# Kernel optimization log

Measured on AMD Instinct MI355X. Metric: run time of the kernel, lower is better.

The kernel has to match this reference:

```python
import jax, jax.numpy as jnp
import numpy as np

B, S1, S2 = 16, 256, 512          # batch, vision len, text len
V_HID, T_HID = 1024, 768          # v_hidden_size, hidden_size
BI_HID, H = 1024, 8               # bi_hidden_size, bi_num_attention_heads
D = BI_HID // H                   # attention_head_size = 128


def setup_inputs() -> dict:
    key = jax.random.key(0)
    ks = jax.random.split(key, 16)
    s = 0.02
    inp = {
        "input_tensor1": jax.random.normal(ks[0], (B, S1, V_HID), jnp.float32),
        "attention_mask1": jnp.zeros((B, 1, 1, S1), jnp.float32),
        "input_tensor2": jax.random.normal(ks[1], (B, S2, T_HID), jnp.float32),
        "attention_mask2": jnp.zeros((B, 1, 1, S2), jnp.float32),
        # vision-stream projections (query1/key1/value1): v_hidden -> all_head_size
        "Wq1": jax.random.normal(ks[2], (V_HID, BI_HID), jnp.float32) * s,
        "bq1": jnp.zeros((BI_HID,), jnp.float32),
        "Wk1": jax.random.normal(ks[3], (V_HID, BI_HID), jnp.float32) * s,
        "bk1": jnp.zeros((BI_HID,), jnp.float32),
        "Wv1": jax.random.normal(ks[4], (V_HID, BI_HID), jnp.float32) * s,
        "bv1": jnp.zeros((BI_HID,), jnp.float32),
        # text-stream projections (query2/key2/value2): hidden -> all_head_size
        "Wq2": jax.random.normal(ks[5], (T_HID, BI_HID), jnp.float32) * s,
        "bq2": jnp.zeros((BI_HID,), jnp.float32),
        "Wk2": jax.random.normal(ks[6], (T_HID, BI_HID), jnp.float32) * s,
        "bk2": jnp.zeros((BI_HID,), jnp.float32),
        "Wv2": jax.random.normal(ks[7], (T_HID, BI_HID), jnp.float32) * s,
        "bv2": jnp.zeros((BI_HID,), jnp.float32),
    }
    return inp


def _heads(x):
    # [B, S, H*D] -> [B, S, H, D]
    b, s, _ = x.shape
    return x.reshape(b, s, H, D)


def reference(input_tensor1, attention_mask1, input_tensor2, attention_mask2,
              Wq1, bq1, Wk1, bk1, Wv1, bv1,
              Wq2, bq2, Wk2, bk2, Wv2, bv2):
    scale = 1.0 / jnp.sqrt(jnp.asarray(D, input_tensor1.dtype))
    # stream 1 (vision) QKV
    q1 = _heads(input_tensor1 @ Wq1 + bq1)
    k1 = _heads(input_tensor1 @ Wk1 + bk1)
    v1 = _heads(input_tensor1 @ Wv1 + bv1)
    # stream 2 (text) QKV
    q2 = _heads(input_tensor2 @ Wq2 + bq2)
    k2 = _heads(input_tensor2 @ Wk2 + bk2)
    v2 = _heads(input_tensor2 @ Wv2 + bv2)

    # attention 1: text queries attend to vision keys/values  -> context1 [B,S2,BI_HID]
    scores1 = jnp.einsum('bqhd,bkhd->bhqk', q2, k1) * scale + attention_mask1
    probs1 = jax.nn.softmax(scores1, axis=-1)  # dropout prob = 0 (eval)
    context1 = jnp.einsum('bhqk,bkhd->bqhd', probs1, v1).reshape(B, S2, BI_HID)

    # attention 2: vision queries attend to text keys/values  -> context2 [B,S1,BI_HID]
    scores2 = jnp.einsum('bqhd,bkhd->bhqk', q1, k2) * scale + attention_mask2
    probs2 = jax.nn.softmax(scores2, axis=-1)
    context2 = jnp.einsum('bhqk,bkhd->bqhd', probs2, v2).reshape(B, S1, BI_HID)

    return (context1, context2)
```

## Files before the change

kernel.cpp:

```cpp
#include <hip/hip_runtime.h>


typedef _Float16 f16;
typedef unsigned int u32;
typedef f16  v8h __attribute__((ext_vector_type(8)));
typedef float v4f __attribute__((ext_vector_type(4)));

struct alignas(8) h4 { f16 x, y, z, w; };

#define GLL16(g, l) __builtin_amdgcn_global_load_lds(                          \
    (const __attribute__((address_space(1))) u32*)(g),                         \
    (__attribute__((address_space(3))) u32*)(l), 16, 0, 0)

#define MFMA16 __builtin_amdgcn_mfma_f32_16x16x32_f16

__global__ __launch_bounds__(256)
void cvt_in(const float* __restrict__ p1, long n1,
            const float* __restrict__ p2, long n2,
            f16* __restrict__ d1, f16* __restrict__ d2)
{
    long i = ((long)blockIdx.x * 256 + threadIdx.x) * 8;
    const float* s; f16* d;
    if (i < n1) { s = p1 + i; d = d1 + i; }
    else        { long j = i - n1; if (j >= n2) return; s = p2 + j; d = d2 + j; }
    float4 a = *(const float4*)s, b = *(const float4*)(s + 4);
    v8h o = {(f16)a.x, (f16)a.y, (f16)a.z, (f16)a.w,
             (f16)b.x, (f16)b.y, (f16)b.z, (f16)b.w};
    *(v8h*)d = o;
}

__global__ __launch_bounds__(256)
void cvt_wT(const float* __restrict__ w0, const float* __restrict__ w1,
            const float* __restrict__ w2, const float* __restrict__ w3,
            const float* __restrict__ w4, const float* __restrict__ w5,
            f16* __restrict__ o1, f16* __restrict__ o2)
{
    const int z = blockIdx.z;
    const int K = z < 3 ? 1024 : 768;
    const int bk = blockIdx.y * 64;
    if (bk >= K) return;
    const float* src = z == 0 ? w0 : z == 1 ? w1 : z == 2 ? w2
                     : z == 3 ? w3 : z == 4 ? w4 : w5;
    f16* dst = z < 3 ? o1 + (size_t)z * 1024 * 1024
                     : o2 + (size_t)(z - 3) * 1024 * 768;

    __shared__ float t[64][65];
    const int bn = blockIdx.x * 64;
    const int r0 = threadIdx.x >> 4, c4 = (threadIdx.x & 15) * 4;
#pragma unroll
    for (int rr = 0; rr < 64; rr += 16) {
        float4 v = *(const float4*)&src[(long)(bk + rr + r0) * 1024 + bn + c4];
        t[rr + r0][c4 + 0] = v.x; t[rr + r0][c4 + 1] = v.y;
        t[rr + r0][c4 + 2] = v.z; t[rr + r0][c4 + 3] = v.w;
    }
    __syncthreads();
#pragma unroll
    for (int rr = 0; rr < 64; rr += 16) {
        const int n = rr + r0;
        h4 o = {(f16)t[c4 + 0][n], (f16)t[c4 + 1][n],
                (f16)t[c4 + 2][n], (f16)t[c4 + 3][n]};
        *(h4*)&dst[(long)(bn + n) * K + bk + c4] = o;
    }
}

__global__ __launch_bounds__(256, 4)
void mm_proj(const f16* __restrict__ A2, const f16* __restrict__ B2,
             const float* __restrict__ bq2, const float* __restrict__ bk2,
             const float* __restrict__ bv2,
             f16* __restrict__ q2o, f16* __restrict__ k2o, f16* __restrict__ v2o,
             const f16* __restrict__ A1, const f16* __restrict__ B1,
             const float* __restrict__ bq1, const float* __restrict__ bk1,
             const float* __restrict__ bv1,
             f16* __restrict__ q1o, f16* __restrict__ k1o, f16* __restrict__ v1o)
{
    __shared__ f16 sh[16384];

    const int gid = blockIdx.x;
    const bool is2 = gid < 1536;
    const int id   = is2 ? gid : gid - 1536;
    const int K    = is2 ? 768 : 1024;
    const int S    = is2 ? 512 : 256;
    const int mdiv = is2 ? 8 : 4;
    const f16* A  = is2 ? A2 : A1;
    const f16* Bw = is2 ? B2 : B1;

    const int by = (id & 7) * mdiv + ((id >> 3) % mdiv);
    const int bx = id / (8 * mdiv);
    const int m0 = by * 128, n0 = bx * 128;

    const int tid = threadIdx.x, lane = tid & 63, w = tid >> 6;
    const int wm = w >> 1, wn = w & 1;
    const int fr = lane & 15, fq = lane >> 4;

    int aoff[4], boff[4];
#pragma unroll
    for (int t = 0; t < 4; ++t) {
        const int ra = wm * 64 + t * 16 + fr;
        aoff[t] = ra * 32 + (fq ^ ((ra >> 1) & 3)) * 8;
        const int rb = wn * 64 + t * 16 + fr;
        boff[t] = rb * 32 + (fq ^ ((rb >> 1) & 3)) * 8;
    }

    auto stage = [&](int k0, int p) {
        f16* Ad = sh + p * 4096;
        f16* Bd = sh + 8192 + p * 4096;
#pragma unroll
        for (int j = 0; j < 2; ++j) {
            const int c = j * 256 + tid, row = c >> 2;
            const int kl = (c & 3) ^ ((row >> 1) & 3);
            GLL16(A  + (long)(m0 + row) * K + k0 + kl * 8, Ad + c * 8);
            GLL16(Bw + (long)(n0 + row) * K + k0 + kl * 8, Bd + c * 8);
        }
    };

    v4f acc[4][4];
#pragma unroll
    for (int i = 0; i < 4; ++i)
#pragma unroll
        for (int j = 0; j < 4; ++j) acc[i][j] = (v4f){0.f, 0.f, 0.f, 0.f};

    stage(0, 0);
    const int NK = K >> 5;
    for (int kt = 0; kt < NK; ++kt) {
        __syncthreads();
        if (kt + 1 < NK) stage((kt + 1) << 5, (kt + 1) & 1);
        const f16* As = sh + (kt & 1) * 4096;
        const f16* Bs = sh + 8192 + (kt & 1) * 4096;
        v8h ah[4], bh[4];
#pragma unroll
        for (int t = 0; t < 4; ++t) ah[t] = *(const v8h*)&As[aoff[t]];
#pragma unroll
        for (int t = 0; t < 4; ++t) bh[t] = *(const v8h*)&Bs[boff[t]];
#pragma unroll
        for (int tmi = 0; tmi < 4; ++tmi)
#pragma unroll
            for (int tni = 0; tni < 4; ++tni)
                acc[tmi][tni] = MFMA16(ah[tmi], bh[tni], acc[tmi][tni], 0, 0, 0);
    }

    const int col = lane & 15, quad = lane >> 4;
    const int seg = n0 >> 10, nbase = n0 & 1023;
    f16* buf = sh;

    if (seg < 2) {
        const float* bias = seg == 0 ? (is2 ? bq2 : bq1) : (is2 ? bk2 : bk1);
        f16* Co = seg == 0 ? (is2 ? q2o : q1o) : (is2 ? k2o : k1o);
#pragma unroll
        for (int pass = 0; pass < 2; ++pass) {
            __syncthreads();
            if (wm == pass) {
#pragma unroll
                for (int tmi = 0; tmi < 4; ++tmi) {
                    const int ml = tmi * 16 + quad * 4;
#pragma unroll
                    for (int tni = 0; tni < 4; ++tni) {
                        const int nl = wn * 64 + tni * 16 + col;
                        const float bvl = bias[nbase + nl];
#pragma unroll
                        for (int i = 0; i < 4; ++i)
                            buf[(ml + i) * 136 + nl] = (f16)(acc[tmi][tni][i] + bvl);
                    }
                }
            }
            __syncthreads();
            const int rr = tid >> 2, cc = (tid & 3) * 32;
            const long gb = (long)(m0 + pass * 64 + rr) * 1024 + nbase + cc;
#pragma unroll
            for (int c = 0; c < 4; ++c)
                *(v8h*)&Co[gb + c * 8] = *(const v8h*)&buf[rr * 136 + cc + c * 8];
        }
    } else {
        const float* bias = is2 ? bv2 : bv1;
        f16* vo = is2 ? v2o : v1o;
        const int bb = m0 / S, s0 = m0 % S;
#pragma unroll
        for (int pass = 0; pass < 2; ++pass) {
            __syncthreads();
            if (wn == pass) {
#pragma unroll
                for (int tmi = 0; tmi < 4; ++tmi) {
                    const int ml = wm * 64 + tmi * 16 + quad * 4;
#pragma unroll
                    for (int tni = 0; tni < 4; ++tni) {
                        const int nl = tni * 16 + col;
                        const float bvl = bias[nbase + pass * 64 + nl];
                        h4 o = {(f16)(acc[tmi][tni][0] + bvl),
                                (f16)(acc[tmi][tni][1] + bvl),
                                (f16)(acc[tmi][tni][2] + bvl),
                                (f16)(acc[tmi][tni][3] + bvl)};
                        *(h4*)&buf[nl * 136 + ml] = o;
                    }
                }
            }
            __syncthreads();
            const int nn = tid >> 2, mm = (tid & 3) * 32;
            const long gb = ((long)bb * 1024 + nbase + pass * 64 + nn) * S + s0 + mm;
#pragma unroll
            for (int c = 0; c < 4; ++c)
                *(v8h*)&vo[gb + c * 8] = *(const v8h*)&buf[nn * 136 + mm + c * 8];
        }
    }
}

__global__ __launch_bounds__(256, 2)
void flash(const f16* __restrict__ q2, const f16* __restrict__ k1,
           const f16* __restrict__ v1, const float* __restrict__ m1,
           float* __restrict__ o1,
           const f16* __restrict__ q1, const f16* __restrict__ k2,
           const f16* __restrict__ v2, const float* __restrict__ m2,
           float* __restrict__ o2, float scale)
{
    constexpr int PSTR = 72;
    __shared__ f16 lds[16384 + 128 * PSTR];
    f16* KL = lds;
    f16* VL = lds + 8192;
    f16* PL = lds + 16384;

    const int gid = blockIdx.x;
    const bool ph2 = gid < 256;
    const int id = ph2 ? gid : gid - 256;
    const int Sq = ph2 ? 256 : 512, Sk = ph2 ? 512 : 256;
    const f16* qp = ph2 ? q1 : q2;
    const f16* kp = ph2 ? k2 : k1;
    const f16* vp = ph2 ? v2 : v1;
    const float* mask = ph2 ? m2 : m1;
    float* out = ph2 ? o2 : o1;

    const int zz = id & 127, yy = id >> 7;
    const int b = zz >> 3, hd = zz & 7;
    const int q0 = yy * 128;
    const int tid = threadIdx.x, lane = tid & 63, w = tid >> 6;
    const int col = lane & 15, quad = lane >> 4;

    v8h qf[2][4];
#pragma unroll
    for (int rt = 0; rt < 2; ++rt) {
        const long qr = ((long)b * Sq + q0 + w * 32 + rt * 16 + col) * 1024
                        + (long)hd * 128;
#pragma unroll
        for (int kf = 0; kf < 4; ++kf)
            qf[rt][kf] = *(const v8h*)(qp + qr + kf * 32 + quad * 8);
    }

    v8h ones;
#pragma unroll
    for (int i = 0; i < 8; ++i) ones[i] = (f16)1.0f;

    v4f O[2][8], Lc[2];
#pragma unroll
    for (int rt = 0; rt < 2; ++rt) {
#pragma unroll
        for (int nj = 0; nj < 8; ++nj) O[rt][nj] = (v4f){0.f, 0.f, 0.f, 0.f};
        Lc[rt] = (v4f){0.f, 0.f, 0.f, 0.f};
    }

    const long kbase = (long)b * Sk * 1024 + (long)hd * 128;
    const long vbase = ((long)b * 1024 + hd * 128) * (long)Sk;
    const int nk = Sk >> 6;

    auto stageK = [&](int kt) {
#pragma unroll
        for (int j = 0; j < 4; ++j) {
            const int c = j * 256 + tid, row = c >> 4, ch = (c & 15) ^ (row & 15);
            GLL16(kp + kbase + (long)(kt * 64 + row) * 1024 + ch * 8, KL + c * 8);
        }
    };
    auto stageV = [&](int kt) {
#pragma unroll
        for (int j = 0; j < 4; ++j) {
            const int c = j * 256 + tid, row = c >> 3, ch = (c & 7) ^ (row & 7);
            GLL16(vp + vbase + (long)row * Sk + kt * 64 + ch * 8, VL + c * 8);
        }
    };

    stageK(0);
    stageV(0);

    float mv[4];
#pragma unroll
    for (int tn = 0; tn < 4; ++tn)
        mv[tn] = mask[(long)b * Sk + tn * 16 + col];

    for (int kt = 0; kt < nk; ++kt) {
        asm volatile("s_waitcnt vmcnt(4)" ::: "memory");
        __builtin_amdgcn_sched_barrier(0);
        __builtin_amdgcn_s_barrier();

        v4f sa[2][4];
#pragma unroll
        for (int rt = 0; rt < 2; ++rt)
#pragma unroll
            for (int tn = 0; tn < 4; ++tn) sa[rt][tn] = (v4f){0.f, 0.f, 0.f, 0.f};
#pragma unroll
        for (int kf = 0; kf < 4; ++kf) {
            v8h bh[4];
#pragma unroll
            for (int tn = 0; tn < 4; ++tn) {
                const int row = tn * 16 + col;
                bh[tn] = *(const v8h*)&KL[row * 128 + ((kf * 4 + quad) ^ (row & 15)) * 8];
            }
            __builtin_amdgcn_s_setprio(1);
#pragma unroll
            for (int rt = 0; rt < 2; ++rt)
#pragma unroll
                for (int tn = 0; tn < 4; ++tn)
                    sa[rt][tn] = MFMA16(qf[rt][kf], bh[tn], sa[rt][tn], 0, 0, 0);
            __builtin_amdgcn_s_setprio(0);
        }

        float mvn[4];
        if (kt + 1 < nk) {
#pragma unroll
            for (int tn = 0; tn < 4; ++tn)
                mvn[tn] = mask[(long)b * Sk + (kt + 1) * 64 + tn * 16 + col];
        }

        asm volatile("s_waitcnt lgkmcnt(0)" ::: "memory");
        __builtin_amdgcn_sched_barrier(0);
        __builtin_amdgcn_s_barrier();
        if (kt + 1 < nk) stageK(kt + 1);

#pragma unroll
        for (int rt = 0; rt < 2; ++rt)
#pragma unroll
            for (int tn = 0; tn < 4; ++tn)
#pragma unroll
                for (int r = 0; r < 4; ++r) {
                    const float p = __expf(sa[rt][tn][r] * scale + mv[tn]);
                    PL[(w * 32 + rt * 16 + quad * 4 + r) * PSTR + tn * 16 + col]
                        = (f16)p;
                }

        if (kt + 1 < nk) asm volatile("s_waitcnt vmcnt(4)" ::: "memory");
        else             asm volatile("s_waitcnt vmcnt(0)" ::: "memory");
        __builtin_amdgcn_sched_barrier(0);
        __builtin_amdgcn_s_barrier();

#pragma unroll
        for (int kf2 = 0; kf2 < 2; ++kf2) {
            v8h vb[8];
#pragma unroll
            for (int nj = 0; nj < 8; ++nj) {
                const int row = nj * 16 + col;
                vb[nj] = *(const v8h*)&VL[row * 64 + ((kf2 * 4 + quad) ^ (row & 7)) * 8];
            }
#pragma unroll
            for (int rt = 0; rt < 2; ++rt) {
                const v8h pa = *(const v8h*)&PL[(w * 32 + rt * 16 + col) * PSTR
                                                + kf2 * 32 + quad * 8];
                __builtin_amdgcn_s_setprio(1);
#pragma unroll
                for (int nj = 0; nj < 8; ++nj)
                    O[rt][nj] = MFMA16(pa, vb[nj], O[rt][nj], 0, 0, 0);
                Lc[rt] = MFMA16(pa, ones, Lc[rt], 0, 0, 0);
                __builtin_amdgcn_s_setprio(0);
            }
        }

        asm volatile("s_waitcnt lgkmcnt(0)" ::: "memory");
        __builtin_amdgcn_sched_barrier(0);
        __builtin_amdgcn_s_barrier();
        if (kt + 1 < nk) stageV(kt + 1);

#pragma unroll
        for (int tn = 0; tn < 4; ++tn) mv[tn] = mvn[tn];
    }

#pragma unroll
    for (int rt = 0; rt < 2; ++rt) {
        float inv[4];
#pragma unroll
        for (int r = 0; r < 4; ++r) inv[r] = 1.0f / Lc[rt][r];
        const long ob = ((long)b * Sq + q0 + w * 32 + rt * 16 + quad * 4) * 1024
                        + (long)hd * 128;
#pragma unroll
        for (int nj = 0; nj < 8; ++nj)
#pragma unroll
            for (int r = 0; r < 4; ++r)
                out[ob + (long)r * 1024 + nj * 16 + col] = O[rt][nj][r] * inv[r];
    }
}

extern "C" void kernel_launch(void* const* d_in, const int* in_sizes, int n_in,
                              void* d_out, int out_size, void* d_ws, size_t ws_size,
                              hipStream_t stream)
{
    const float* in1   = (const float*)d_in[0];
    const float* mask1 = (const float*)d_in[1];
    const float* in2   = (const float*)d_in[2];
    const float* mask2 = (const float*)d_in[3];
    const float* Wq1 = (const float*)d_in[4];  const float* bq1 = (const float*)d_in[5];
    const float* Wk1 = (const float*)d_in[6];  const float* bk1 = (const float*)d_in[7];
    const float* Wv1 = (const float*)d_in[8];  const float* bv1 = (const float*)d_in[9];
    const float* Wq2 = (const float*)d_in[10]; const float* bq2 = (const float*)d_in[11];
    const float* Wk2 = (const float*)d_in[12]; const float* bk2 = (const float*)d_in[13];
    const float* Wv2 = (const float*)d_in[14]; const float* bv2 = (const float*)d_in[15];

    constexpr int Bb = 16, S1 = 256, S2 = 512, VH = 1024, TH = 768;
    constexpr long M1 = (long)Bb * S1, M2 = (long)Bb * S2;
    const float scale = 0.088388347648318447f;

    f16* W = (f16*)d_ws;
    f16* i1  = W;
    f16* i2  = i1 + M1 * VH;
    f16* w1  = i2 + M2 * TH;
    f16* w2  = w1 + (long)3072 * VH;
    f16* q1  = w2 + (long)3072 * TH;
    f16* k1  = q1 + M1 * 1024;
    f16* v1t = k1 + M1 * 1024;
    f16* q2  = v1t + M1 * 1024;
    f16* k2  = q2 + M2 * 1024;
    f16* v2t = k2 + M2 * 1024;
    float* out = (float*)d_out;

    cvt_in<<<dim3(5120), 256, 0, stream>>>(in1, M1 * VH, in2, M2 * TH, i1, i2);
    cvt_wT<<<dim3(16, 16, 6), 256, 0, stream>>>(Wq1, Wk1, Wv1, Wq2, Wk2, Wv2, w1, w2);

    mm_proj<<<dim3(2304), 256, 0, stream>>>(
        i2, w2, bq2, bk2, bv2, q2, k2, v2t,
        i1, w1, bq1, bk1, bv1, q1, k1, v1t);

    flash<<<dim3(768), 256, 0, stream>>>(
        q2, k1, v1t, mask1, out,
        q1, k2, v2t, mask2, out + M2 * 1024, scale);
}
```

Measured before the change: 252.5 us.

## Enlarge projection GEMM tile to 256x128, single-buffer LDS, merge conversion kernels

The two fp32-to-fp16 conversion kernels (inputs and transposed weights) are merged into one launch, dispatching on block index. The projection GEMM tile grows from 128x128 to 256x128, giving each warp 8x4 MFMA accumulators and halving the block count. LDS staging moves from double-buffered to single-buffered with a sync before compute. The intent is more operand reuse per tile and one fewer launch, but the change also gives up load/compute overlap and raises register pressure.

Measured after the change: 602.0 us. 2.38x slower.

```diff
diff --git a/kernel.cpp b/kernel.cpp
--- a/kernel.cpp
+++ b/kernel.cpp
@@ -15,37 +15,39 @@
 #define MFMA16 __builtin_amdgcn_mfma_f32_16x16x32_f16
 
 __global__ __launch_bounds__(256)
-void cvt_in(const float* __restrict__ p1, long n1,
-            const float* __restrict__ p2, long n2,
-            f16* __restrict__ d1, f16* __restrict__ d2)
+void cvt_all(const float* __restrict__ p1, long n1,
+             const float* __restrict__ p2, long n2,
+             f16* __restrict__ d1, f16* __restrict__ d2,
+             const float* __restrict__ w0, const float* __restrict__ w1,
+             const float* __restrict__ w2, const float* __restrict__ w3,
+             const float* __restrict__ w4, const float* __restrict__ w5,
+             f16* __restrict__ o1, f16* __restrict__ o2)
 {
-    long i = ((long)blockIdx.x * 256 + threadIdx.x) * 8;
-    const float* s; f16* d;
-    if (i < n1) { s = p1 + i; d = d1 + i; }
-    else        { long j = i - n1; if (j >= n2) return; s = p2 + j; d = d2 + j; }
-    float4 a = *(const float4*)s, b = *(const float4*)(s + 4);
-    v8h o = {(f16)a.x, (f16)a.y, (f16)a.z, (f16)a.w,
-             (f16)b.x, (f16)b.y, (f16)b.z, (f16)b.w};
-    *(v8h*)d = o;
-}
-
-__global__ __launch_bounds__(256)
-void cvt_wT(const float* __restrict__ w0, const float* __restrict__ w1,
-            const float* __restrict__ w2, const float* __restrict__ w3,
-            const float* __restrict__ w4, const float* __restrict__ w5,
-            f16* __restrict__ o1, f16* __restrict__ o2)
-{
-    const int z = blockIdx.z;
+    __shared__ float t[64][65];
+    const int bid = blockIdx.x;
+    if (bid < 5120) {
+        long i = ((long)bid * 256 + threadIdx.x) * 8;
+        const float* s; f16* d;
+        if (i < n1) { s = p1 + i; d = d1 + i; }
+        else        { long j = i - n1; if (j >= n2) return; s = p2 + j; d = d2 + j; }
+        float4 a = *(const float4*)s, b = *(const float4*)(s + 4);
+        v8h o = {(f16)a.x, (f16)a.y, (f16)a.z, (f16)a.w,
+                 (f16)b.x, (f16)b.y, (f16)b.z, (f16)b.w};
+        *(v8h*)d = o;
+        return;
+    }
+    const int id = bid - 5120;
+    const int z = id >> 8;
+    const int rem = id & 255;
     const int K = z < 3 ? 1024 : 768;
-    const int bk = blockIdx.y * 64;
+    const int bk = (rem >> 4) * 64;
     if (bk >= K) return;
     const float* src = z == 0 ? w0 : z == 1 ? w1 : z == 2 ? w2
                      : z == 3 ? w3 : z == 4 ? w4 : w5;
     f16* dst = z < 3 ? o1 + (size_t)z * 1024 * 1024
                      : o2 + (size_t)(z - 3) * 1024 * 768;
 
-    __shared__ float t[64][65];
-    const int bn = blockIdx.x * 64;
+    const int bn = (rem & 15) * 64;
     const int r0 = threadIdx.x >> 4, c4 = (threadIdx.x & 15) * 4;
 #pragma unroll
     for (int rr = 0; rr < 64; rr += 16) {
@@ -64,140 +66,145 @@
 }
 
 __global__ __launch_bounds__(256, 4)
-void mm_proj(const f16* __restrict__ A2, const f16* __restrict__ B2,
+void mm_proj(const f16* __restrict__ A1, const f16* __restrict__ B1,
+             const float* __restrict__ bq1, const float* __restrict__ bk1,
+             const float* __restrict__ bv1,
+             f16* __restrict__ q1o, f16* __restrict__ k1o, f16* __restrict__ v1o,
+             const f16* __restrict__ A2, const f16* __restrict__ B2,
              const float* __restrict__ bq2, const float* __restrict__ bk2,
              const float* __restrict__ bv2,
-             f16* __restrict__ q2o, f16* __restrict__ k2o, f16* __restrict__ v2o,
-             const f16* __restrict__ A1, const f16* __restrict__ B1,
-             const float* __restrict__ bq1, const float* __restrict__ bk1,
-             const float* __restrict__ bv1,
-             f16* __restrict__ q1o, f16* __restrict__ k1o, f16* __restrict__ v1o)
+             f16* __restrict__ q2o, f16* __restrict__ k2o, f16* __restrict__ v2o)
 {
-    __shared__ f16 sh[16384];
+    __shared__ f16 sh[17408];
 
     const int gid = blockIdx.x;
-    const bool is2 = gid < 1536;
-    const int id   = is2 ? gid : gid - 1536;
-    const int K    = is2 ? 768 : 1024;
-    const int S    = is2 ? 512 : 256;
-    const int mdiv = is2 ? 8 : 4;
-    const f16* A  = is2 ? A2 : A1;
-    const f16* Bw = is2 ? B2 : B1;
-
-    const int by = (id & 7) * mdiv + ((id >> 3) % mdiv);
-    const int bx = id / (8 * mdiv);
-    const int m0 = by * 128, n0 = bx * 128;
+    const bool is1 = gid < 384;
+    const int id   = is1 ? gid : gid - 384;
+    const int K    = is1 ? 1024 : 768;
+    const int S    = is1 ? 256 : 512;
+    int by, bx;
+    if (is1) { by = (id & 7) * 2 + ((id >> 3) & 1); bx = id >> 4; }
+    else     { by = (id & 7) * 4 + ((id >> 3) & 3); bx = id >> 5; }
+    const int m0 = by << 8, n0 = bx << 7;
+    const f16* A  = is1 ? A1 : A2;
+    const f16* Bw = is1 ? B1 : B2;
 
     const int tid = threadIdx.x, lane = tid & 63, w = tid >> 6;
     const int wm = w >> 1, wn = w & 1;
     const int fr = lane & 15, fq = lane >> 4;
 
-    int aoff[4], boff[4];
-#pragma unroll
-    for (int t = 0; t < 4; ++t) {
-        const int ra = wm * 64 + t * 16 + fr;
-        aoff[t] = ra * 32 + (fq ^ ((ra >> 1) & 3)) * 8;
-        const int rb = wn * 64 + t * 16 + fr;
-        boff[t] = rb * 32 + (fq ^ ((rb >> 1) & 3)) * 8;
-    }
-
-    auto stage = [&](int k0, int p) {
-        f16* Ad = sh + p * 4096;
-        f16* Bd = sh + 8192 + p * 4096;
+    int aoff[8], boff[4];
+#pragma unroll
+    for (int mi = 0; mi < 8; ++mi) {
+        const int ra = wm * 128 + mi * 16 + fr;
+        aoff[mi] = ra * 32 + (fq ^ ((ra >> 1) & 3)) * 8;
+    }
+#pragma unroll
+    for (int n = 0; n < 4; ++n) {
+        const int rb = wn * 64 + n * 16 + fr;
+        boff[n] = rb * 32 + (fq ^ ((rb >> 1) & 3)) * 8;
+    }
+
+    auto stage = [&](int k0) {
+#pragma unroll
+        for (int j = 0; j < 4; ++j) {
+            const int c = j * 256 + tid, row = c >> 2;
+            const int kl = (c & 3) ^ ((row >> 1) & 3);
+            GLL16(A + (long)(m0 + row) * K + k0 + kl * 8, sh + c * 8);
+        }
 #pragma unroll
         for (int j = 0; j < 2; ++j) {
             const int c = j * 256 + tid, row = c >> 2;
             const int kl = (c & 3) ^ ((row >> 1) & 3);
-            GLL16(A  + (long)(m0 + row) * K + k0 + kl * 8, Ad + c * 8);
-            GLL16(Bw + (long)(n0 + row) * K + k0 + kl * 8, Bd + c * 8);
+            GLL16(Bw + (long)(n0 + row) * K + k0 + kl * 8, sh + 8192 + c * 8);
         }
     };
 
-    v4f acc[4][4];
-#pragma unroll
-    for (int i = 0; i < 4; ++i)
+    v4f acc[8][4];
+#pragma unroll
+    for (int i = 0; i < 8; ++i)
 #pragma unroll
         for (int j = 0; j < 4; ++j) acc[i][j] = (v4f){0.f, 0.f, 0.f, 0.f};
 
-    stage(0, 0);
     const int NK = K >> 5;
     for (int kt = 0; kt < NK; ++kt) {
         __syncthreads();
-        if (kt + 1 < NK) stage((kt + 1) << 5, (kt + 1) & 1);
-        const f16* As = sh + (kt & 1) * 4096;
-        const f16* Bs = sh + 8192 + (kt & 1) * 4096;
-        v8h ah[4], bh[4];
-#pragma unroll
-        for (int t = 0; t < 4; ++t) ah[t] = *(const v8h*)&As[aoff[t]];
-#pragma unroll
-        for (int t = 0; t < 4; ++t) bh[t] = *(const v8h*)&Bs[boff[t]];
-#pragma unroll
-        for (int tmi = 0; tmi < 4; ++tmi)
-#pragma unroll
-            for (int tni = 0; tni < 4; ++tni)
-                acc[tmi][tni] = MFMA16(ah[tmi], bh[tni], acc[tmi][tni], 0, 0, 0);
-    }
-
-    const int col = lane & 15, quad = lane >> 4;
+        stage(kt << 5);
+        __syncthreads();
+        v8h bh[4];
+#pragma unroll
+        for (int n = 0; n < 4; ++n) bh[n] = *(const v8h*)&sh[8192 + boff[n]];
+#pragma unroll
+        for (int mi = 0; mi < 8; ++mi) {
+            const v8h ah = *(const v8h*)&sh[aoff[mi]];
+#pragma unroll
+            for (int n = 0; n < 4; ++n)
+                acc[mi][n] = MFMA16(ah, bh[n], acc[mi][n], 0, 0, 0);
+        }
+    }
+
+    const int col = fr, quad = lane >> 4;
     const int seg = n0 >> 10, nbase = n0 & 1023;
     f16* buf = sh;
 
     if (seg < 2) {
-        const float* bias = seg == 0 ? (is2 ? bq2 : bq1) : (is2 ? bk2 : bk1);
-        f16* Co = seg == 0 ? (is2 ? q2o : q1o) : (is2 ? k2o : k1o);
+        const float* bias = seg == 0 ? (is1 ? bq1 : bq2) : (is1 ? bk1 : bk2);
+        f16* Co = seg == 0 ? (is1 ? q1o : q2o) : (is1 ? k1o : k2o);
+        float bl[4];
+#pragma unroll
+        for (int n = 0; n < 4; ++n) bl[n] = bias[nbase + wn * 64 + n * 16 + col];
 #pragma unroll
         for (int pass = 0; pass < 2; ++pass) {
             __syncthreads();
             if (wm == pass) {
 #pragma unroll
-                for (int tmi = 0; tmi < 4; ++tmi) {
-                    const int ml = tmi * 16 + quad * 4;
-#pragma unroll
-                    for (int tni = 0; tni < 4; ++tni) {
-                        const int nl = wn * 64 + tni * 16 + col;
-                        const float bvl = bias[nbase + nl];
+                for (int mi = 0; mi < 8; ++mi) {
+                    const int ml = mi * 16 + quad * 4;
+#pragma unroll
+                    for (int n = 0; n < 4; ++n) {
+                        const int nl = wn * 64 + n * 16 + col;
 #pragma unroll
                         for (int i = 0; i < 4; ++i)
-                            buf[(ml + i) * 136 + nl] = (f16)(acc[tmi][tni][i] + bvl);
+                            buf[(ml + i) * 136 + nl] = (f16)(acc[mi][n][i] + bl[n]);
                     }
                 }
             }
             __syncthreads();
-            const int rr = tid >> 2, cc = (tid & 3) * 32;
-            const long gb = (long)(m0 + pass * 64 + rr) * 1024 + nbase + cc;
-#pragma unroll
-            for (int c = 0; c < 4; ++c)
+            const int rr = tid >> 1, cc = (tid & 1) * 64;
+            const long gb = (long)(m0 + pass * 128 + rr) * 1024 + nbase + cc;
+#pragma unroll
+            for (int c = 0; c < 8; ++c)
                 *(v8h*)&Co[gb + c * 8] = *(const v8h*)&buf[rr * 136 + cc + c * 8];
         }
     } else {
-        const float* bias = is2 ? bv2 : bv1;
-        f16* vo = is2 ? v2o : v1o;
+        const float* bias = is1 ? bv1 : bv2;
+        f16* vo = is1 ? v1o : v2o;
         const int bb = m0 / S, s0 = m0 % S;
 #pragma unroll
         for (int pass = 0; pass < 2; ++pass) {
             __syncthreads();
             if (wn == pass) {
 #pragma unroll
-                for (int tmi = 0; tmi < 4; ++tmi) {
-                    const int ml = wm * 64 + tmi * 16 + quad * 4;
-#pragma unroll
-                    for (int tni = 0; tni < 4; ++tni) {
-                        const int nl = tni * 16 + col;
+                for (int mi = 0; mi < 8; ++mi) {
+                    const int ml = wm * 128 + mi * 16 + quad * 4;
+#pragma unroll
+                    for (int n = 0; n < 4; ++n) {
+                        const int nl = n * 16 + col;
                         const float bvl = bias[nbase + pass * 64 + nl];
-                        h4 o = {(f16)(acc[tmi][tni][0] + bvl),
-                                (f16)(acc[tmi][tni][1] + bvl),
-                                (f16)(acc[tmi][tni][2] + bvl),
-                                (f16)(acc[tmi][tni][3] + bvl)};
-                        *(h4*)&buf[nl * 136 + ml] = o;
+                        h4 o = {(f16)(acc[mi][n][0] + bvl),
+                                (f16)(acc[mi][n][1] + bvl),
+                                (f16)(acc[mi][n][2] + bvl),
+                                (f16)(acc[mi][n][3] + bvl)};
+                        *(h4*)&buf[nl * 264 + ml] = o;
                     }
                 }
             }
             __syncthreads();
-            const int nn = tid >> 2, mm = (tid & 3) * 32;
+            const int nn = tid >> 2, mm = (tid & 3) * 64;
             const long gb = ((long)bb * 1024 + nbase + pass * 64 + nn) * S + s0 + mm;
 #pragma unroll
-            for (int c = 0; c < 4; ++c)
-                *(v8h*)&vo[gb + c * 8] = *(const v8h*)&buf[nn * 136 + mm + c * 8];
+            for (int c = 0; c < 8; ++c)
+                *(v8h*)&vo[gb + c * 8] = *(const v8h*)&buf[nn * 264 + mm + c * 8];
         }
     }
 }
@@ -413,12 +420,13 @@
     f16* v2t = k2 + M2 * 1024;
     float* out = (float*)d_out;
 
-    cvt_in<<<dim3(5120), 256, 0, stream>>>(in1, M1 * VH, in2, M2 * TH, i1, i2);
-    cvt_wT<<<dim3(16, 16, 6), 256, 0, stream>>>(Wq1, Wk1, Wv1, Wq2, Wk2, Wv2, w1, w2);
-
-    mm_proj<<<dim3(2304), 256, 0, stream>>>(
-        i2, w2, bq2, bk2, bv2, q2, k2, v2t,
-        i1, w1, bq1, bk1, bv1, q1, k1, v1t);
+    cvt_all<<<dim3(6656), 256, 0, stream>>>(
+        in1, M1 * VH, in2, M2 * TH, i1, i2,
+        Wq1, Wk1, Wv1, Wq2, Wk2, Wv2, w1, w2);
+
+    mm_proj<<<dim3(1152), 256, 0, stream>>>(
+        i1, w1, bq1, bk1, bv1, q1, k1, v1t,
+        i2, w2, bq2, bk2, bv2, q2, k2, v2t);
 
     flash<<<dim3(768), 256, 0, stream>>>(
         q2, k1, v1t, mask1, out,
```
